# Optimization experiments

Hardware: AMD Instinct MI355X
Metric: run time of the kernel (lower is better)

Reference implementation:

```python
import jax, jax.numpy as jnp
import numpy as np

N = 100000   # nodes
E = 640000   # edges
H = 8        # attention heads
C = 16       # hidden_channels (per-head out dim)
IN = 4       # in_channels
G = 64       # graphs in the batch
NE = 2       # num_experts
HC = H * C   # 128 = concat feature width
SLOPE = 0.2  # GATConv leaky_relu negative slope


def _p(k, shape):
    return 0.1 * jax.random.normal(k, shape, jnp.float32)


def setup_inputs() -> dict:
    key = jax.random.key(0)
    ks = jax.random.split(key, 32)
    inp = {
        "x": jax.random.normal(ks[0], (N, IN), jnp.float32),
        "edge_index": jax.random.randint(ks[1], (2, E), 0, N),
        "edge_attr": jax.random.normal(ks[2], (E, 1), jnp.float32),
        "batch": jnp.sort(jax.random.randint(ks[3], (N,), 0, G)),
    }
    i = 4
    for l, d in zip((1, 2, 3), (IN, HC, HC)):
        inp[f"w{l}"] = _p(ks[i], (d, HC)); i += 1      # node lin
        inp[f"as{l}"] = _p(ks[i], (H, C)); i += 1      # att_src
        inp[f"ad{l}"] = _p(ks[i], (H, C)); i += 1      # att_dst
        inp[f"we{l}"] = _p(ks[i], (1, HC)); i += 1     # lin_edge
        inp[f"ae{l}"] = _p(ks[i], (H, C)); i += 1      # att_edge
        inp[f"b{l}"] = jnp.zeros((HC,), jnp.float32)
    inp["fw1"] = _p(ks[i], (HC, 4 * C)); inp["fb1"] = jnp.zeros((4 * C,), jnp.float32)
    inp["fw2"] = _p(ks[i + 1], (4 * C, NE)); inp["fb2"] = jnp.zeros((NE,), jnp.float32)
    return inp


def gat_layer(x, src, dst, eattr, w, a_s, a_d, we, a_e, b):
    """PyG GATConv (concat=True, edge_dim=1): gather-attend-segment_softmax-scatter."""
    n = x.shape[0]
    h = (x @ w).reshape(n, H, C)                       # [N,H,C]
    alpha_src = jnp.sum(h * a_s, axis=-1)              # [N,H]
    alpha_dst = jnp.sum(h * a_d, axis=-1)              # [N,H]
    ef = (eattr @ we).reshape(-1, H, C)                # [E,H,C]
    alpha_e = jnp.sum(ef * a_e, axis=-1)               # [E,H]
    alpha = jax.nn.leaky_relu(alpha_src[src] + alpha_dst[dst] + alpha_e, SLOPE)
    # segment softmax over incoming edges of each dst node
    m = jax.lax.stop_gradient(jax.ops.segment_max(alpha, dst, num_segments=n))
    m = jnp.where(jnp.isfinite(m), m, 0.0)
    ex = jnp.exp(alpha - m[dst])
    den = jax.ops.segment_sum(ex, dst, num_segments=n)
    alpha = ex / (den[dst] + 1e-16)
    out = jax.ops.segment_sum(h[src] * alpha[:, :, None], dst, num_segments=n)
    return out.reshape(n, HC) + b


def add_self_loops_mean(src, dst, eattr, n):
    """add_self_loops(fill_value='mean'): self-loop attr = mean of incoming edge attrs."""
    cnt = jax.ops.segment_sum(jnp.ones(src.shape, eattr.dtype), dst, num_segments=n)
    loop = jax.ops.segment_sum(eattr, dst, num_segments=n) / jnp.maximum(cnt, 1.0)[:, None]
    idx = jnp.arange(n, dtype=src.dtype)
    return (jnp.concatenate([src, idx]), jnp.concatenate([dst, idx]),
            jnp.concatenate([eattr, loop], axis=0))


def reference(x, edge_index, edge_attr, batch,
              w1, as1, ad1, we1, ae1, b1,
              w2, as2, ad2, we2, ae2, b2,
              w3, as3, ad3, we3, ae3, b3,
              fw1, fb1, fw2, fb2):
    src, dst = edge_index[0], edge_index[1]
    # conv1: add_self_loops=False
    h = jax.nn.relu(gat_layer(x, src, dst, edge_attr, w1, as1, ad1, we1, ae1, b1))
    # conv2/conv3: default add_self_loops=True with fill_value='mean'
    s2, d2, e2 = add_self_loops_mean(src, dst, edge_attr, x.shape[0])
    h = jax.nn.relu(gat_layer(h, s2, d2, e2, w2, as2, ad2, we2, ae2, b2))
    h = jax.nn.relu(gat_layer(h, s2, d2, e2, w3, as3, ad3, we3, ae3, b3))
    # global mean pool over `batch`
    gsum = jax.ops.segment_sum(h, batch, num_segments=G)
    cnt = jax.ops.segment_sum(jnp.ones((h.shape[0],), h.dtype), batch, num_segments=G)
    emb = gsum / jnp.maximum(cnt, 1.0)[:, None]
    gh = jax.nn.relu(emb @ fw1 + fb1)
    return gh @ fw2 + fb2
```

## Files before the change

### kernel.cpp

```cpp
#include <hip/hip_runtime.h>
#include <hip/hip_bf16.h>
#include <math.h>

#define NHEAD 8
#define CDIM 16
#define HCDIM 128
#define NGRAPH 64
#define WEXT 144
#define SWPAD 136

typedef __attribute__((ext_vector_type(8))) short short8;
typedef __attribute__((ext_vector_type(4))) float f32x4;

static __device__ __forceinline__ unsigned short f2bf(float f) {
    unsigned u = __float_as_uint(f);
    unsigned r = (u + 0x7FFF + ((u >> 16) & 1)) >> 16;
    return (unsigned short)r;
}
static __device__ __forceinline__ float bf2f(unsigned short s) {
    return __uint_as_float(((unsigned)s) << 16);
}


__global__ void setup0(int* __restrict__ deg,
                       float* __restrict__ gsum,
                       const float* __restrict__ w2, const float* __restrict__ w3,
                       unsigned short* __restrict__ wt2, unsigned short* __restrict__ wt3,
                       const float* __restrict__ we1, const float* __restrict__ ae1,
                       const float* __restrict__ we2, const float* __restrict__ ae2,
                       const float* __restrict__ we3, const float* __restrict__ ae3,
                       float* __restrict__ kc,
                       const float* __restrict__ as2, const float* __restrict__ ad2,
                       const float* __restrict__ as3, const float* __restrict__ ad3,
                       const float* __restrict__ w1,
                       const float* __restrict__ as1, const float* __restrict__ ad1,
                       float* __restrict__ wastab, float* __restrict__ wadtab,
                       const int* __restrict__ batch, int* __restrict__ gstart, int n) {
    int i = blockIdx.x * 256 + threadIdx.x;
    if (i < n) deg[i] = 0;
    if (i < NGRAPH * HCDIM) gsum[i] = 0.f;
    if (i < WEXT * HCDIM) {
        int nn = i >> 7, k = i & 127;
        float v2, v3;
        if (nn < HCDIM) {
            v2 = w2[k * HCDIM + nn];
            v3 = w3[k * HCDIM + nn];
        } else if (nn < HCDIM + NHEAD) {
            int h = nn - HCDIM;
            float s2 = 0.f, s3 = 0.f;
#pragma unroll
            for (int c = 0; c < CDIM; ++c) {
                s2 += w2[k * HCDIM + h * CDIM + c] * as2[h * CDIM + c];
                s3 += w3[k * HCDIM + h * CDIM + c] * as3[h * CDIM + c];
            }
            v2 = s2; v3 = s3;
        } else {
            int h = nn - HCDIM - NHEAD;
            float s2 = 0.f, s3 = 0.f;
#pragma unroll
            for (int c = 0; c < CDIM; ++c) {
                s2 += w2[k * HCDIM + h * CDIM + c] * ad2[h * CDIM + c];
                s3 += w3[k * HCDIM + h * CDIM + c] * ad3[h * CDIM + c];
            }
            v2 = s2; v3 = s3;
        }
        wt2[nn * HCDIM + k] = f2bf(v2);
        wt3[nn * HCDIM + k] = f2bf(v3);
    }
    if (i < 24) {
        int l = i >> 3, h = i & 7;
        const float* we = (l == 0) ? we1 : ((l == 1) ? we2 : we3);
        const float* ae = (l == 0) ? ae1 : ((l == 1) ? ae2 : ae3);
        float s = 0.f;
        for (int c = 0; c < CDIM; ++c) s += we[h * CDIM + c] * ae[h * CDIM + c];
        kc[i] = s;
    }
    if (i >= 18560 && i <= 18560 + NGRAPH) {
        int g = i - 18560;
        int lo = 0, hi = n;
        while (lo < hi) {
            int mid = (lo + hi) >> 1;
            if (batch[mid] < g) lo = mid + 1; else hi = mid;
        }
        gstart[g] = lo;
    }
    if (i >= 18700 && i < 18732) {
        int t = i - 18700;
        int k = t >> 3, h = t & 7;
        float ss = 0.f, sd = 0.f;
#pragma unroll
        for (int c = 0; c < CDIM; ++c) {
            ss += w1[k * HCDIM + h * CDIM + c] * as1[h * CDIM + c];
            sd += w1[k * HCDIM + h * CDIM + c] * ad1[h * CDIM + c];
        }
        wastab[t] = ss;
        wadtab[t] = sd;
    }
}

__global__ void count_deg(const int* __restrict__ dst, int* __restrict__ deg,
                          int* __restrict__ erank, int E) {
    int e = blockIdx.x * 256 + threadIdx.x;
    if (e >= E) return;
    erank[e] = atomicAdd(&deg[dst[e]], 1);
}

__global__ __launch_bounds__(512) void block_sum(const int* __restrict__ deg,
                                                 int* __restrict__ bsum, int n) {
    __shared__ int s[512];
    int i = blockIdx.x * 512 + threadIdx.x;
    s[threadIdx.x] = (i < n) ? deg[i] : 0;
    __syncthreads();
    for (int off = 256; off > 0; off >>= 1) {
        if (threadIdx.x < off) s[threadIdx.x] += s[threadIdx.x + off];
        __syncthreads();
    }
    if (threadIdx.x == 0) bsum[blockIdx.x] = s[0];
}

__global__ __launch_bounds__(512) void scan_final2(const int* __restrict__ deg,
                                                   const int* __restrict__ bsum, int nb,
                                                   int* __restrict__ eoff, int n) {
    __shared__ int ls[512];
    __shared__ int s[512];
    const int t = threadIdx.x;
    ls[t] = (t < nb) ? bsum[t] : 0;
    int i = blockIdx.x * 512 + t;
    s[t] = (i < n) ? deg[i] : 0;
    __syncthreads();
    for (int off = 1; off < 512; off <<= 1) {
        int a1 = (t >= off) ? ls[t - off] : 0;
        int a2 = (t >= off) ? s[t - off] : 0;
        __syncthreads();
        ls[t] += a1; s[t] += a2;
        __syncthreads();
    }
    int base = (blockIdx.x > 0) ? ls[blockIdx.x - 1] : 0;
    if (i < n) eoff[i + 1] = base + s[t];
    if (i == 0) eoff[0] = 0;
}

__global__ void scatter_edges(const int* __restrict__ src, const int* __restrict__ dst,
                              const float* __restrict__ eattr,
                              const int* __restrict__ eoff,
                              const int* __restrict__ erank,
                              int2* __restrict__ epack, int E) {
    int e = blockIdx.x * 256 + threadIdx.x;
    if (e >= E) return;
    int p = eoff[dst[e]] + erank[e];
    epack[p] = make_int2(src[e], __float_as_int(eattr[e]));
}


__global__ __launch_bounds__(256) void gat_aggregate1(
    const float* __restrict__ x,
    const int2*  __restrict__ epack,
    const int*   __restrict__ eoff,
    const float* __restrict__ w1,
    const float* __restrict__ wastab,
    const float* __restrict__ wadtab,
    const float* __restrict__ kc,
    const float* __restrict__ bias,
    unsigned short* __restrict__ outbf,
    int n) {
    const int lane = threadIdx.x & 63;
    const int hl = lane & 31;
    int nid = ((blockIdx.x * 256 + threadIdx.x) >> 6) * 2 + (lane >> 5);
    if (nid >= n) return;
    const int h = hl >> 2;
    const int c0 = hl * 4;

    float was0 = wastab[0 * NHEAD + h], was1_ = wastab[1 * NHEAD + h];
    float was2 = wastab[2 * NHEAD + h], was3 = wastab[3 * NHEAD + h];
    float wad0 = wadtab[0 * NHEAD + h], wad1_ = wadtab[1 * NHEAD + h];
    float wad2 = wadtab[2 * NHEAD + h], wad3 = wadtab[3 * NHEAD + h];

    float4 xd = *(const float4*)(x + (long)nid * 4);
    const float adst_h = xd.x * wad0 + xd.y * wad1_ + xd.z * wad2 + xd.w * wad3;
    const float k_h = kc[h];
    const int e0 = eoff[nid], e1 = eoff[nid + 1];

    float den = 0.f;
    float a0 = 0.f, a1 = 0.f, a2 = 0.f, a3 = 0.f;

    for (int base = e0; base < e1; base += 4) {
        int2 ep[4];
#pragma unroll
        for (int j = 0; j < 4; ++j) {
            int idx = base + j; idx = (idx < e1) ? idx : (e1 - 1);
            ep[j] = epack[idx];
        }
        float4 xs[4];
#pragma unroll
        for (int j = 0; j < 4; ++j) xs[j] = *(const float4*)(x + (long)ep[j].x * 4);
#pragma unroll
        for (int j = 0; j < 4; ++j) {
            bool valid = (base + j < e1);
            float as_e = xs[j].x * was0 + xs[j].y * was1_ + xs[j].z * was2 + xs[j].w * was3;
            float a = as_e + adst_h + __int_as_float(ep[j].y) * k_h;
            a = (a > 0.f) ? a : 0.2f * a;
            float w = valid ? __expf(a) : 0.f;
            den += w;
            a0 += xs[j].x * w; a1 += xs[j].y * w;
            a2 += xs[j].z * w; a3 += xs[j].w * w;
        }
    }

    float inv = 1.f / (den + 1e-16f);
    float4 wk0 = *(const float4*)(w1 + 0 * HCDIM + c0);
    float4 wk1 = *(const float4*)(w1 + 1 * HCDIM + c0);
    float4 wk2 = *(const float4*)(w1 + 2 * HCDIM + c0);
    float4 wk3 = *(const float4*)(w1 + 3 * HCDIM + c0);
    float4 bv = *(const float4*)(bias + c0);
    float o0 = fmaxf((a0 * wk0.x + a1 * wk1.x + a2 * wk2.x + a3 * wk3.x) * inv + bv.x, 0.f);
    float o1 = fmaxf((a0 * wk0.y + a1 * wk1.y + a2 * wk2.y + a3 * wk3.y) * inv + bv.y, 0.f);
    float o2 = fmaxf((a0 * wk0.z + a1 * wk1.z + a2 * wk2.z + a3 * wk3.z) * inv + bv.z, 0.f);
    float o3 = fmaxf((a0 * wk0.w + a1 * wk1.w + a2 * wk2.w + a3 * wk3.w) * inv + bv.w, 0.f);
    ushort4 hv = make_ushort4(f2bf(o0), f2bf(o1), f2bf(o2), f2bf(o3));
    *(ushort4*)(outbf + (long)nid * HCDIM + c0) = hv;
}


__global__ __launch_bounds__(256) void gemm_mfma(const unsigned short* __restrict__ A,
                                                 const unsigned short* __restrict__ Wt,
                                                 unsigned short* __restrict__ Ybf,
                                                 float* __restrict__ asrcn,
                                                 float* __restrict__ adstn, int n) {
    __shared__ unsigned short sW[WEXT][SWPAD];
    for (int i = threadIdx.x; i < WEXT * 16; i += 256) {
        int r = i >> 4, c = (i & 15) << 3;
        *(short8*)&sW[r][c] = *(const short8*)(Wt + r * HCDIM + c);
    }
    __syncthreads();

    const int wave = threadIdx.x >> 6;
    const int lane = threadIdx.x & 63;
    const int quad = lane >> 4;
    const int l16  = lane & 15;
    const int rowbase = (blockIdx.x * 8 + wave * 2) * 16;

    f32x4 acc[2][9];
#pragma unroll
    for (int r = 0; r < 2; ++r)
#pragma unroll
        for (int t = 0; t < 9; ++t) acc[r][t] = (f32x4){0.f, 0.f, 0.f, 0.f};

#pragma unroll
    for (int kb = 0; kb < HCDIM; kb += 32) {
        short8 a[2];
#pragma unroll
        for (int r = 0; r < 2; ++r) {
            int row = rowbase + r * 16 + l16;
            row = (row < n) ? row : (n - 1);
            a[r] = *(const short8*)(A + (long)row * HCDIM + kb + quad * 8);
        }
#pragma unroll
        for (int nt = 0; nt < 9; ++nt) {
            short8 b = *(const short8*)(&sW[nt * 16 + l16][kb + quad * 8]);
#pragma unroll
            for (int r = 0; r < 2; ++r)
                acc[r][nt] = __builtin_amdgcn_mfma_f32_16x16x32_bf16(a[r], b, acc[r][nt], 0, 0, 0);
        }
    }

#pragma unroll
    for (int r = 0; r < 2; ++r) {
#pragma unroll
        for (int reg = 0; reg < 4; ++reg) {
            int row = rowbase + r * 16 + quad * 4 + reg;
            if (row < n) {
                unsigned short* yp = Ybf + (long)row * HCDIM + l16;
#pragma unroll
                for (int nt = 0; nt < 8; ++nt) yp[nt * 16] = f2bf(acc[r][nt][reg]);
                float cv = acc[r][8][reg];
                if (l16 < 8) asrcn[row * NHEAD + l16] = cv;
                else         adstn[row * NHEAD + (l16 - 8)] = cv;
            }
        }
    }
}


__global__ __launch_bounds__(256) void gat_aggregate(
    const unsigned short* __restrict__ hlin,
    const float* __restrict__ asrc,
    const float* __restrict__ adst,
    const int2*  __restrict__ epack,
    const int*   __restrict__ eoff,
    const float* __restrict__ kc,
    const float* __restrict__ bias,
    float* __restrict__ outf,
    unsigned short* __restrict__ outbf,
    int n, int use_loop, int split_out) {
    const int lane = threadIdx.x & 63;
    const int hl = lane & 31;
    int nid = ((blockIdx.x * 256 + threadIdx.x) >> 6) * 2 + (lane >> 5);
    if (nid >= n) return;
    const int h = hl >> 2;
    const int c0 = hl * 4;

    const float adst_h = adst[nid * NHEAD + h];
    const float k_h = kc[h];
    const int e0 = eoff[nid], e1 = eoff[nid + 1];

    float den = 0.f, sume = 0.f;
    float ax = 0.f, ay = 0.f, az = 0.f, aw = 0.f;

    for (int base = e0; base < e1; base += 4) {
        int2 ep[4];
#pragma unroll
        for (int j = 0; j < 4; ++j) {
            int idx = base + j; idx = (idx < e1) ? idx : (e1 - 1);
            ep[j] = epack[idx];
        }
        float av[4]; ushort4 hv[4];
#pragma unroll
        for (int j = 0; j < 4; ++j) {
            av[j] = asrc[ep[j].x * NHEAD + h];
            hv[j] = *(const ushort4*)(hlin + (long)ep[j].x * HCDIM + c0);
        }
#pragma unroll
        for (int j = 0; j < 4; ++j) {
            bool valid = (base + j < e1);
            float ea = __int_as_float(ep[j].y);
            float a = av[j] + adst_h + ea * k_h;
            a = (a > 0.f) ? a : 0.2f * a;
            float w = valid ? __expf(a) : 0.f;
            sume += valid ? ea : 0.f;
            den += w;
            ax += bf2f(hv[j].x) * w; ay += bf2f(hv[j].y) * w;
            az += bf2f(hv[j].z) * w; aw += bf2f(hv[j].w) * w;
        }
    }

    if (use_loop) {
        float fl = sume / fmaxf((float)(e1 - e0), 1.f);
        float a = asrc[nid * NHEAD + h] + adst_h + fl * k_h;
        a = (a > 0.f) ? a : 0.2f * a;
        float w = __expf(a);
        ushort4 hv = *(const ushort4*)(hlin + (long)nid * HCDIM + c0);
        den += w;
        ax += bf2f(hv.x) * w; ay += bf2f(hv.y) * w;
        az += bf2f(hv.z) * w; aw += bf2f(hv.w) * w;
    }

    float inv = 1.f / (den + 1e-16f);
    float4 bv = *(const float4*)(bias + c0);
    float o0 = fmaxf(ax * inv + bv.x, 0.f);
    float o1 = fmaxf(ay * inv + bv.y, 0.f);
    float o2 = fmaxf(az * inv + bv.z, 0.f);
    float o3 = fmaxf(aw * inv + bv.w, 0.f);
    if (split_out) {
        ushort4 hv = make_ushort4(f2bf(o0), f2bf(o1), f2bf(o2), f2bf(o3));
        *(ushort4*)(outbf + (long)nid * HCDIM + c0) = hv;
    } else {
        *(float4*)(outf + (long)nid * HCDIM + c0) = make_float4(o0, o1, o2, o3);
    }
}


__global__ __launch_bounds__(128) void pool_seg(const float* __restrict__ H,
                                                const int* __restrict__ gstart,
                                                float* __restrict__ gsum) {
    const int c = threadIdx.x;
    const int g = blockIdx.x >> 3;
    const int chunk = blockIdx.x & 7;
    int s0 = gstart[g], s1 = gstart[g + 1];
    int len = s1 - s0;
    if (len <= 0) return;
    int cl = (len + 7) >> 3;
    int i0 = s0 + chunk * cl;
    int i1 = min(i0 + cl, s1);
    if (i0 >= i1) return;
    float acc = 0.f;
    int i = i0;
    for (; i + 4 <= i1; i += 4) {
        float v0 = H[(long)i * HCDIM + c];
        float v1 = H[(long)(i + 1) * HCDIM + c];
        float v2 = H[(long)(i + 2) * HCDIM + c];
        float v3 = H[(long)(i + 3) * HCDIM + c];
        acc += (v0 + v1) + (v2 + v3);
    }
    for (; i < i1; ++i) acc += H[(long)i * HCDIM + c];
    atomicAdd(&gsum[g * HCDIM + c], acc);
}

__global__ __launch_bounds__(64) void mlp_kernel(const float* __restrict__ gsum,
                                                 const int* __restrict__ gstart,
                                                 const float* __restrict__ fw1,
                                                 const float* __restrict__ fb1,
                                                 const float* __restrict__ fw2,
                                                 const float* __restrict__ fb2,
                                                 float* __restrict__ out) {
    const int g = blockIdx.x;
    const int j = threadIdx.x;
    __shared__ float emb[HCDIM];
    __shared__ float gh[64];
    int cnt = gstart[g + 1] - gstart[g];
    float invc = 1.f / fmaxf((float)cnt, 1.f);
    emb[j] = gsum[g * HCDIM + j] * invc;
    emb[j + 64] = gsum[g * HCDIM + 64 + j] * invc;
    __syncthreads();
    float a = fb1[j];
    for (int k = 0; k < HCDIM; ++k) a += emb[k] * fw1[k * 64 + j];
    gh[j] = fmaxf(a, 0.f);
    __syncthreads();
    if (j < 2) {
        float o = fb2[j];
        for (int k = 0; k < 64; ++k) o += gh[k] * fw2[k * 2 + j];
        out[g * 2 + j] = o;
    }
}


extern "C" void kernel_launch(void* const* d_in, const int* in_sizes, int n_in,
                              void* d_out, int out_size, void* d_ws, size_t ws_size,
                              hipStream_t stream) {
    const float* x     = (const float*)d_in[0];
    const int*   eidx  = (const int*)d_in[1];
    const float* eattr = (const float*)d_in[2];
    const int*   batch = (const int*)d_in[3];
    const float* w1  = (const float*)d_in[4];
    const float* as1 = (const float*)d_in[5];
    const float* ad1 = (const float*)d_in[6];
    const float* we1 = (const float*)d_in[7];
    const float* ae1 = (const float*)d_in[8];
    const float* b1  = (const float*)d_in[9];
    const float* w2  = (const float*)d_in[10];
    const float* as2 = (const float*)d_in[11];
    const float* ad2 = (const float*)d_in[12];
    const float* we2 = (const float*)d_in[13];
    const float* ae2 = (const float*)d_in[14];
    const float* b2  = (const float*)d_in[15];
    const float* w3  = (const float*)d_in[16];
    const float* as3 = (const float*)d_in[17];
    const float* ad3 = (const float*)d_in[18];
    const float* we3 = (const float*)d_in[19];
    const float* ae3 = (const float*)d_in[20];
    const float* b3  = (const float*)d_in[21];
    const float* fw1 = (const float*)d_in[22];
    const float* fb1 = (const float*)d_in[23];
    const float* fw2 = (const float*)d_in[24];
    const float* fb2 = (const float*)d_in[25];

    const int N = in_sizes[3];
    const int E = in_sizes[2];
    const int* src = eidx;
    const int* dst = eidx + E;

    char* p = (char*)d_ws;
    auto alloc = [&](size_t bytes) {
        void* r = (void*)p;
        p += (bytes + 255) & ~(size_t)255;
        return r;
    };
    unsigned short* Abf = (unsigned short*)alloc((size_t)N * HCDIM * 2);
    char*  Bbuf   = (char*)alloc((size_t)N * HCDIM * 4);
    unsigned short* Bbf = (unsigned short*)Bbuf;
    float* Bf32   = (float*)Bbuf;
    float* asrcA  = (float*)alloc((size_t)N * NHEAD * 4);
    float* adstA  = (float*)alloc((size_t)N * NHEAD * 4);
    float* asrcB  = (float*)alloc((size_t)N * NHEAD * 4);
    float* adstB  = (float*)alloc((size_t)N * NHEAD * 4);
    int*   deg    = (int*)alloc((size_t)N * 4);
    int*   eoff   = (int*)alloc((size_t)(N + 1) * 4);
    int*   erank  = (int*)alloc((size_t)E * 4);
    int2*  epack  = (int2*)alloc((size_t)E * 8);
    int*   bsum   = (int*)alloc(((size_t)(N + 511) / 512) * 4);
    float* kc     = (float*)alloc(24 * 4);
    int*   gstart = (int*)alloc((NGRAPH + 1) * 4);
    float* gsum   = (float*)alloc(NGRAPH * HCDIM * 4);
    float* wastab = (float*)alloc(32 * 4);
    float* wadtab = (float*)alloc(32 * 4);
    unsigned short* wt2 = (unsigned short*)alloc(WEXT * HCDIM * 2);
    unsigned short* wt3 = (unsigned short*)alloc(WEXT * HCDIM * 2);

    const int NB = (N + 255) / 256;
    const int NB512 = (N + 511) / 512;
    const int EB = (E + 255) / 256;
    const int AGG_BLOCKS = (((N + 1) / 2) * 64 + 255) / 256;
    const int GEMM_BLOCKS = (N + 127) / 128;

    setup0<<<NB, 256, 0, stream>>>(deg, gsum,
                                   w2, w3, wt2, wt3,
                                   we1, ae1, we2, ae2, we3, ae3, kc,
                                   as2, ad2, as3, ad3,
                                   w1, as1, ad1, wastab, wadtab,
                                   batch, gstart, N);
    count_deg<<<EB, 256, 0, stream>>>(dst, deg, erank, E);
    block_sum<<<NB512, 512, 0, stream>>>(deg, bsum, N);
    scan_final2<<<NB512, 512, 0, stream>>>(deg, bsum, NB512, eoff, N);
    scatter_edges<<<EB, 256, 0, stream>>>(src, dst, eattr, eoff, erank, epack, E);

    gat_aggregate1<<<AGG_BLOCKS, 256, 0, stream>>>(x, epack, eoff, w1, wastab, wadtab,
                                                   kc + 0, b1, Bbf, N);
    gemm_mfma<<<GEMM_BLOCKS, 256, 0, stream>>>(Bbf, wt2, Abf, asrcB, adstB, N);
    gat_aggregate<<<AGG_BLOCKS, 256, 0, stream>>>(Abf, asrcB, adstB, epack, eoff,
                                                  kc + 8, b2, Bf32, Bbf, N, 1, 1);
    gemm_mfma<<<GEMM_BLOCKS, 256, 0, stream>>>(Bbf, wt3, Abf, asrcA, adstA, N);
    gat_aggregate<<<AGG_BLOCKS, 256, 0, stream>>>(Abf, asrcA, adstA, epack, eoff,
                                                  kc + 16, b3, Bf32, Bbf, N, 1, 0);

    pool_seg<<<NGRAPH * 8, 128, 0, stream>>>(Bf32, gstart, gsum);
    mlp_kernel<<<NGRAPH, 64, 0, stream>>>(gsum, gstart, fw1, fb1, fw2, fb2, (float*)d_out);
}
```

Baseline: 347.7 us.

## Use 16 lanes per node with 8-wide bf16 gathers; store final layer as bf16

The aggregation kernels now give each node 16 lanes instead of 32, with each lane handling 8 channels through a 16-byte short8 load. A wave therefore covers 4 nodes, which halves the redundant per-edge index and attention loads and doubles the bytes per gather instruction. The last GAT layer now writes bf16 instead of fp32, and pooling reads bf16, halving that write and read traffic. The cost is more registers per lane, fewer lanes in flight per node, and bf16 rounding before pooling.

Result: faster. 326.2 us (-6.2%).

```diff
diff --git a/kernel.cpp b/kernel.cpp
--- a/kernel.cpp
+++ b/kernel.cpp
@@ -164,11 +164,11 @@
     unsigned short* __restrict__ outbf,
     int n) {
     const int lane = threadIdx.x & 63;
-    const int hl = lane & 31;
-    int nid = ((blockIdx.x * 256 + threadIdx.x) >> 6) * 2 + (lane >> 5);
+    const int l16 = lane & 15;
+    int nid = ((blockIdx.x * 256 + threadIdx.x) >> 6) * 4 + (lane >> 4);
     if (nid >= n) return;
-    const int h = hl >> 2;
-    const int c0 = hl * 4;
+    const int h = l16 >> 1;
+    const int c0 = l16 * 8;
 
     float was0 = wastab[0 * NHEAD + h], was1_ = wastab[1 * NHEAD + h];
     float was2 = wastab[2 * NHEAD + h], was3 = wastab[3 * NHEAD + h];
@@ -207,17 +207,15 @@
     }
 
     float inv = 1.f / (den + 1e-16f);
-    float4 wk0 = *(const float4*)(w1 + 0 * HCDIM + c0);
-    float4 wk1 = *(const float4*)(w1 + 1 * HCDIM + c0);
-    float4 wk2 = *(const float4*)(w1 + 2 * HCDIM + c0);
-    float4 wk3 = *(const float4*)(w1 + 3 * HCDIM + c0);
-    float4 bv = *(const float4*)(bias + c0);
-    float o0 = fmaxf((a0 * wk0.x + a1 * wk1.x + a2 * wk2.x + a3 * wk3.x) * inv + bv.x, 0.f);
-    float o1 = fmaxf((a0 * wk0.y + a1 * wk1.y + a2 * wk2.y + a3 * wk3.y) * inv + bv.y, 0.f);
-    float o2 = fmaxf((a0 * wk0.z + a1 * wk1.z + a2 * wk2.z + a3 * wk3.z) * inv + bv.z, 0.f);
-    float o3 = fmaxf((a0 * wk0.w + a1 * wk1.w + a2 * wk2.w + a3 * wk3.w) * inv + bv.w, 0.f);
-    ushort4 hv = make_ushort4(f2bf(o0), f2bf(o1), f2bf(o2), f2bf(o3));
-    *(ushort4*)(outbf + (long)nid * HCDIM + c0) = hv;
+    short8 o;
+#pragma unroll
+    for (int c = 0; c < 8; ++c) {
+        float oc = a0 * w1[0 * HCDIM + c0 + c] + a1 * w1[1 * HCDIM + c0 + c] +
+                   a2 * w1[2 * HCDIM + c0 + c] + a3 * w1[3 * HCDIM + c0 + c];
+        oc = fmaxf(oc * inv + bias[c0 + c], 0.f);
+        o[c] = (short)f2bf(oc);
+    }
+    *(short8*)(outbf + (long)nid * HCDIM + c0) = o;
 }
 
 
@@ -289,22 +287,23 @@
     const int*   __restrict__ eoff,
     const float* __restrict__ kc,
     const float* __restrict__ bias,
-    float* __restrict__ outf,
-    unsigned short* __restrict__ outbf,
-    int n, int use_loop, int split_out) {
+    unsigned short* __restrict__ out,
+    int n, int use_loop) {
     const int lane = threadIdx.x & 63;
-    const int hl = lane & 31;
-    int nid = ((blockIdx.x * 256 + threadIdx.x) >> 6) * 2 + (lane >> 5);
+    const int l16 = lane & 15;
+    int nid = ((blockIdx.x * 256 + threadIdx.x) >> 6) * 4 + (lane >> 4);
     if (nid >= n) return;
-    const int h = hl >> 2;
-    const int c0 = hl * 4;
+    const int h = l16 >> 1;
+    const int c0 = l16 * 8;
 
     const float adst_h = adst[nid * NHEAD + h];
     const float k_h = kc[h];
     const int e0 = eoff[nid], e1 = eoff[nid + 1];
 
     float den = 0.f, sume = 0.f;
-    float ax = 0.f, ay = 0.f, az = 0.f, aw = 0.f;
+    float acc[8];
+#pragma unroll
+    for (int c = 0; c < 8; ++c) acc[c] = 0.f;
 
     for (int base = e0; base < e1; base += 4) {
         int2 ep[4];
@@ -313,11 +312,11 @@
             int idx = base + j; idx = (idx < e1) ? idx : (e1 - 1);
             ep[j] = epack[idx];
         }
-        float av[4]; ushort4 hv[4];
+        float av[4]; short8 hv[4];
 #pragma unroll
         for (int j = 0; j < 4; ++j) {
             av[j] = asrc[ep[j].x * NHEAD + h];
-            hv[j] = *(const ushort4*)(hlin + (long)ep[j].x * HCDIM + c0);
+            hv[j] = *(const short8*)(hlin + (long)ep[j].x * HCDIM + c0);
         }
 #pragma unroll
         for (int j = 0; j < 4; ++j) {
@@ -328,8 +327,9 @@
             float w = valid ? __expf(a) : 0.f;
             sume += valid ? ea : 0.f;
             den += w;
-            ax += bf2f(hv[j].x) * w; ay += bf2f(hv[j].y) * w;
-            az += bf2f(hv[j].z) * w; aw += bf2f(hv[j].w) * w;
+#pragma unroll
+            for (int c = 0; c < 8; ++c)
+                acc[c] += bf2f((unsigned short)hv[j][c]) * w;
         }
     }
 
@@ -338,28 +338,25 @@
         float a = asrc[nid * NHEAD + h] + adst_h + fl * k_h;
         a = (a > 0.f) ? a : 0.2f * a;
         float w = __expf(a);
-        ushort4 hv = *(const ushort4*)(hlin + (long)nid * HCDIM + c0);
+        short8 hv = *(const short8*)(hlin + (long)nid * HCDIM + c0);
         den += w;
-        ax += bf2f(hv.x) * w; ay += bf2f(hv.y) * w;
-        az += bf2f(hv.z) * w; aw += bf2f(hv.w) * w;
+#pragma unroll
+        for (int c = 0; c < 8; ++c)
+            acc[c] += bf2f((unsigned short)hv[c]) * w;
     }
 
     float inv = 1.f / (den + 1e-16f);
-    float4 bv = *(const float4*)(bias + c0);
-    float o0 = fmaxf(ax * inv + bv.x, 0.f);
-    float o1 = fmaxf(ay * inv + bv.y, 0.f);
-    float o2 = fmaxf(az * inv + bv.z, 0.f);
-    float o3 = fmaxf(aw * inv + bv.w, 0.f);
-    if (split_out) {
-        ushort4 hv = make_ushort4(f2bf(o0), f2bf(o1), f2bf(o2), f2bf(o3));
-        *(ushort4*)(outbf + (long)nid * HCDIM + c0) = hv;
-    } else {
-        *(float4*)(outf + (long)nid * HCDIM + c0) = make_float4(o0, o1, o2, o3);
-    }
-}
-
-
-__global__ __launch_bounds__(128) void pool_seg(const float* __restrict__ H,
+    short8 o;
+#pragma unroll
+    for (int c = 0; c < 8; ++c) {
+        float oc = fmaxf(acc[c] * inv + bias[c0 + c], 0.f);
+        o[c] = (short)f2bf(oc);
+    }
+    *(short8*)(out + (long)nid * HCDIM + c0) = o;
+}
+
+
+__global__ __launch_bounds__(128) void pool_seg(const unsigned short* __restrict__ H,
                                                 const int* __restrict__ gstart,
                                                 float* __restrict__ gsum) {
     const int c = threadIdx.x;
@@ -375,13 +372,13 @@
     float acc = 0.f;
     int i = i0;
     for (; i + 4 <= i1; i += 4) {
-        float v0 = H[(long)i * HCDIM + c];
-        float v1 = H[(long)(i + 1) * HCDIM + c];
-        float v2 = H[(long)(i + 2) * HCDIM + c];
-        float v3 = H[(long)(i + 3) * HCDIM + c];
+        float v0 = bf2f(H[(long)i * HCDIM + c]);
+        float v1 = bf2f(H[(long)(i + 1) * HCDIM + c]);
+        float v2 = bf2f(H[(long)(i + 2) * HCDIM + c]);
+        float v3 = bf2f(H[(long)(i + 3) * HCDIM + c]);
         acc += (v0 + v1) + (v2 + v3);
     }
-    for (; i < i1; ++i) acc += H[(long)i * HCDIM + c];
+    for (; i < i1; ++i) acc += bf2f(H[(long)i * HCDIM + c]);
     atomicAdd(&gsum[g * HCDIM + c], acc);
 }
 
@@ -455,9 +452,7 @@
         return r;
     };
     unsigned short* Abf = (unsigned short*)alloc((size_t)N * HCDIM * 2);
-    char*  Bbuf   = (char*)alloc((size_t)N * HCDIM * 4);
-    unsigned short* Bbf = (unsigned short*)Bbuf;
-    float* Bf32   = (float*)Bbuf;
+    unsigned short* Bbf = (unsigned short*)alloc((size_t)N * HCDIM * 2);
     float* asrcA  = (float*)alloc((size_t)N * NHEAD * 4);
     float* adstA  = (float*)alloc((size_t)N * NHEAD * 4);
     float* asrcB  = (float*)alloc((size_t)N * NHEAD * 4);
@@ -478,7 +473,7 @@
     const int NB = (N + 255) / 256;
     const int NB512 = (N + 511) / 512;
     const int EB = (E + 255) / 256;
-    const int AGG_BLOCKS = (((N + 1) / 2) * 64 + 255) / 256;
+    const int AGG_BLOCKS = (((N + 3) / 4) * 64 + 255) / 256;
     const int GEMM_BLOCKS = (N + 127) / 128;
 
     setup0<<<NB, 256, 0, stream>>>(deg, gsum,
@@ -496,11 +491,11 @@
                                                    kc + 0, b1, Bbf, N);
     gemm_mfma<<<GEMM_BLOCKS, 256, 0, stream>>>(Bbf, wt2, Abf, asrcB, adstB, N);
     gat_aggregate<<<AGG_BLOCKS, 256, 0, stream>>>(Abf, asrcB, adstB, epack, eoff,
-                                                  kc + 8, b2, Bf32, Bbf, N, 1, 1);
+                                                  kc + 8, b2, Bbf, N, 1);
     gemm_mfma<<<GEMM_BLOCKS, 256, 0, stream>>>(Bbf, wt3, Abf, asrcA, adstA, N);
     gat_aggregate<<<AGG_BLOCKS, 256, 0, stream>>>(Abf, asrcA, adstA, epack, eoff,
-                                                  kc + 16, b3, Bf32, Bbf, N, 1, 0);
-
-    pool_seg<<<NGRAPH * 8, 128, 0, stream>>>(Bf32, gstart, gsum);
+                                                  kc + 16, b3, Bbf, N, 1);
+
+    pool_seg<<<NGRAPH * 8, 128, 0, stream>>>(Bbf, gstart, gsum);
     mlp_kernel<<<NGRAPH, 64, 0, stream>>>(gsum, gstart, fw1, fb1, fw2, fb2, (float*)d_out);
 }
```
